# Kernel optimization log

Measured on AMD Instinct MI355X. Metric: run time of the kernel, lower is better.

Reference implementation:

```python
import jax, jax.numpy as jnp
import numpy as np
from jax import lax

DIM = 512; HEADS = 8; HD = DIM // HEADS; SM = 16; NS = 3
B = 8; HH = 32; WW = 32; N = HH * WW; HL = DIM // 4


def setup_inputs() -> dict:
    key = jax.random.key(0)
    ks = iter(jax.random.split(key, 64))
    def g(shape, s=0.02):
        return jax.random.normal(next(ks), shape, dtype=jnp.float32) * s
    z = lambda *sh: jnp.zeros(sh, jnp.float32)
    inp = {
        'x': jax.random.normal(next(ks), (B, N, DIM), dtype=jnp.float32),
        'H': HH, 'W': WW,
        'qkv_w': g((NS, 3 * DIM, DIM)),
        'proj_w': g((DIM, DIM)), 'proj_b': z(DIM),
        'pos_sw': g((HEADS, SM, HD, 2)), 'neg_sw': g((HEADS, SM, HD, 2)),
        'spec_mix': jnp.ones((HEADS, SM), jnp.float32),
        'ca_w1': g((DIM // 2, DIM)), 'ca_b1': z(DIM // 2),
        'ca_w2': g((HEADS * 4, DIM // 2)), 'ca_b2': z(HEADS * 4),
        'lstm_wih_f': g((4 * HL, DIM)), 'lstm_whh_f': g((4 * HL, HL)),
        'lstm_bih_f': z(4 * HL), 'lstm_bhh_f': z(4 * HL),
        'lstm_wih_b': g((4 * HL, DIM)), 'lstm_whh_b': g((4 * HL, HL)),
        'lstm_bih_b': z(4 * HL), 'lstm_bhh_b': z(4 * HL),
        'mha_in_w': g((3 * DIM, DIM)), 'mha_in_b': z(3 * DIM),
        'mha_out_w': g((DIM, DIM)), 'mha_out_b': z(DIM),
        'ge_w1': g((DIM // 2, DIM)), 'ge_b1': z(DIM // 2),
        'ge_w2': g((HEADS * 2, DIM // 2)), 'ge_b2': z(HEADS * 2),
        'spw': jnp.ones((NS, HEADS, HD), jnp.float32),
        'dwc_w5': g((HD, 1, 5, 5), 0.05), 'dwc_b5': z(HD),
        'dwc_w7': g((HD, 1, 7, 7), 0.05), 'dwc_b7': z(HD),
        'dwc_w9': g((HD, 1, 9, 9), 0.05), 'dwc_b9': z(HD),
        'mode_w': jnp.ones((3,), jnp.float32) / 3.0,
    }
    return inp


def reference(x, H, W, qkv_w, proj_w, proj_b, pos_sw, neg_sw, spec_mix,
              ca_w1, ca_b1, ca_w2, ca_b2,
              lstm_wih_f, lstm_whh_f, lstm_bih_f, lstm_bhh_f,
              lstm_wih_b, lstm_whh_b, lstm_bih_b, lstm_bhh_b,
              mha_in_w, mha_in_b, mha_out_w, mha_out_b,
              ge_w1, ge_b1, ge_w2, ge_b2, spw,
              dwc_w5, dwc_b5, dwc_w7, dwc_b7, dwc_w9, dwc_b9, mode_w):
    Bn, Nn, C = x.shape
    heads = HEADS; hd = C // heads

    # ---------- DynamicContextEncoder ----------
    def lstm_dir(xs, wih, whh, bih, bhh):
        # xs: (N, B, C); PyTorch gate order i,f,g,o
        gates_x = xs @ wih.T + (bih + bhh)
        hdim = whh.shape[1]
        def step(carry, gx):
            h, c = carry
            gi = gx + h @ whh.T
            i, f, gg, o = jnp.split(gi, 4, axis=-1)
            c = jax.nn.sigmoid(f) * c + jax.nn.sigmoid(i) * jnp.tanh(gg)
            h = jax.nn.sigmoid(o) * jnp.tanh(c)
            return (h, c), h
        z0 = jnp.zeros((xs.shape[1], hdim), xs.dtype)
        _, hs = lax.scan(step, (z0, z0), gates_x)
        return hs

    xs = jnp.swapaxes(x, 0, 1)  # (N, B, C)
    h_f = lstm_dir(xs, lstm_wih_f, lstm_whh_f, lstm_bih_f, lstm_bhh_f)
    h_b = lstm_dir(xs[::-1], lstm_wih_b, lstm_whh_b, lstm_bih_b, lstm_bhh_b)[::-1]
    local_ctx = jnp.concatenate([h_f, h_b], -1).mean(0)  # (B, dim//2)
    local_ctx = jnp.pad(local_ctx, ((0, 0), (0, C - local_ctx.shape[1])))

    nh2 = heads // 2; hd2 = C // nh2
    qkv_c = x @ mha_in_w.T + mha_in_b
    qc, kc, vc = jnp.split(qkv_c, 3, -1)
    sh = lambda t: t.reshape(Bn, Nn, nh2, hd2).transpose(0, 2, 1, 3)
    qc, kc, vc = sh(qc), sh(kc), sh(vc)
    attn = jax.nn.softmax(jnp.einsum('bhnd,bhmd->bhnm', qc, kc) / float(np.sqrt(hd2)), -1)
    ac = jnp.einsum('bhnm,bhmd->bhnd', attn, vc).transpose(0, 2, 1, 3).reshape(Bn, Nn, C)
    ac = ac @ mha_out_w.T + mha_out_b
    combined = x.mean(1) + local_ctx + ac.mean(1)
    coeffs = jax.nn.sigmoid(jax.nn.relu(combined @ ca_w1.T + ca_b1) @ ca_w2.T + ca_b2)
    coeffs = coeffs.reshape(Bn, heads, 4)

    # ---------- GradientInformedMixer coefficients (x_grad is zeros) ----------
    gz = jnp.zeros((Bn, C), x.dtype)
    gmix = jax.nn.softmax((jnp.tanh(gz @ ge_w1.T + ge_b1) @ ge_w2.T + ge_b2).reshape(Bn, heads, 2), -1)

    # ---------- SpectralPolarityMixer ----------
    smix = jax.nn.softmax(spec_mix, -1).mean(-1)[None, :, None, None]  # per-head scalar
    wp = (pos_sw[..., 0] + 1j * pos_sw[..., 1])[:, :SM, :SM]
    wn = (neg_sw[..., 0] + 1j * neg_sw[..., 1])[:, :SM, :SM]

    def spectral(t):
        tf = jnp.fft.rfft2(t)[:, :, :SM, :SM]
        tp = jnp.fft.irfft2(tf * wp[None], s=(Nn, hd))
        tn = jnp.fft.irfft2(tf * wn[None], s=(Nn, hd))
        return tp + tn * smix

    def safe_pow(t, p):  # relu(t)**p with safe grads
        tp = jnp.where(t > 0, t, 1.0)
        return jnp.where(t > 0, tp ** p, 0.0)

    mw = jax.nn.softmax(mode_w, 0)
    def dwc(xi, w, b):
        return lax.conv_general_dilated(xi, w, (1, 1), 'SAME',
                                        feature_group_count=xi.shape[1],
                                        dimension_numbers=('NCHW', 'OIHW', 'NCHW')) + b[None, :, None, None]

    c0, c1, c2, c3 = [coeffs[:, :, i][:, :, None, None] for i in range(4)]
    g0, g1 = gmix[:, :, 0][:, :, None, None], gmix[:, :, 1][:, :, None, None]

    outs = []
    for s in range(NS):
        qkv = (x @ qkv_w[s].T).reshape(Bn, Nn, 3, heads, hd).transpose(2, 0, 3, 1, 4)
        q, k, v = qkv[0], qkv[1], qkv[2]  # (B, heads, N, hd)
        q = spectral(q); k = spectral(k)
        p = (1.0 + jnp.abs(spw[s]))[None, :, None, :]
        q_pos = safe_pow(q, p); q_neg = safe_pow(-q, p)
        k_pos = safe_pow(k, p); k_neg = safe_pow(-k, p)
        kvpp = jnp.einsum('bhnd,bhne->bhde', k_pos, v)
        kvnn = jnp.einsum('bhnd,bhne->bhde', k_neg, v)
        z = (jnp.einsum('bhnd,bhd->bhn', q_pos, k_pos.sum(2))
             + jnp.einsum('bhnd,bhd->bhn', q_neg, k_neg.sum(2)) + 1e-6)[..., None]
        same = (c0 * jnp.einsum('bhnd,bhde->bhne', q_pos, kvpp)
                + c1 * jnp.einsum('bhnd,bhde->bhne', q_neg, kvnn)) / z
        opp = (c2 * jnp.einsum('bhnd,bhde->bhne', q_pos, kvnn)
               + c3 * jnp.einsum('bhnd,bhde->bhne', q_neg, kvpp)) / z
        mixed = g0 * same + g1 * opp
        v_img = v.reshape(Bn * heads, H, W, hd).transpose(0, 3, 1, 2)
        vcv = mw[0] * dwc(v_img, dwc_w5, dwc_b5) + mw[1] * dwc(v_img, dwc_w7, dwc_b7) + mw[2] * dwc(v_img, dwc_w9, dwc_b9)
        vcv = vcv.transpose(0, 2, 3, 1).reshape(Bn, heads, Nn, hd)
        outs.append(mixed + vcv)

    out = jnp.stack(outs).mean(0).transpose(0, 2, 1, 3).reshape(Bn, Nn, C)
    return out @ proj_w.T + proj_b
```

## Files before the change

kernel.cpp:

```cpp
#include <hip/hip_runtime.h>
#include <hip/hip_bf16.h>
#include <math.h>

typedef __bf16 bf16x8 __attribute__((ext_vector_type(8)));
typedef __bf16 bf16x4 __attribute__((ext_vector_type(4)));
typedef float  f32x4  __attribute__((ext_vector_type(4)));
typedef const float __attribute__((address_space(1)))* gf1p;

#define MFMA(a,b,c) __builtin_amdgcn_mfma_f32_16x16x32_bf16(a, b, c, 0, 0, 0)
#define LOG2E 1.4426950408889634f

static constexpr size_t OFF_R0    = 0;
static constexpr size_t OFF_GXT   = 12582912;
static constexpr size_t OFF_ACCUM = OFF_GXT;
static constexpr size_t OFF_FINAL = OFF_GXT + 4194304;
static constexpr size_t SOFF      = OFF_GXT + 8388608;
static constexpr size_t OFF_ROWSUM= SOFF;
static constexpr size_t OFF_COLW  = OFF_ROWSUM + 32768;
static constexpr size_t OFF_BM    = OFF_COLW;
static constexpr size_t OFF_XPART = OFF_COLW + 327680;
static constexpr size_t OFF_ACM   = OFF_COLW + 524288;
static constexpr size_t OFF_XMEAN = OFF_ACM + 4096;
static constexpr size_t OFF_LC    = OFF_XMEAN + 4096;
static constexpr size_t OFF_COEF  = OFF_LC + 2048;
static constexpr size_t OFF_GMIX  = OFF_COEF + 256;
static constexpr size_t OFF_MW    = OFF_GMIX + 16;
static constexpr size_t OFF_CONV9 = OFF_MW + 4;
static constexpr size_t OFF_CBIAS = OFF_CONV9 + 5184;
static constexpr size_t OFF_WEFF  = OFF_CBIAS + 64;
static constexpr size_t OFF_PPOW  = OFF_WEFF + 4096;
static constexpr size_t OFF_LBIAS = OFF_PPOW + 1536;
static constexpr size_t OFF_W2    = OFF_LBIAS + 1024;
static constexpr size_t OFF_W1CS  = OFF_W2 + 2048;
static constexpr size_t OFF_W1T   = OFF_W1CS + 16384;
static constexpr size_t OFF_HB    = OFF_W1T + 16384;
static constexpr size_t OFF_XB    = OFF_FINAL;
static constexpr size_t OFF_QW    = OFF_FINAL + 2097152;
static constexpr size_t OFF_MW2   = OFF_FINAL + 3276800;
static constexpr size_t OFF_WFB   = OFF_FINAL + 3670016;
static constexpr size_t OFF_WBB   = OFF_FINAL + 3801088;
static constexpr size_t OFF_PWB   = OFF_FINAL + 3932160;

__device__ __forceinline__ float sigm(float x){ return __builtin_amdgcn_rcpf(1.0f + exp2f(-LOG2E*x)); }
__device__ __forceinline__ float tanhx(float x){ return 2.0f*__builtin_amdgcn_rcpf(1.0f + exp2f(-2.0f*LOG2E*x)) - 1.0f; }
__device__ __forceinline__ unsigned pk2(float a, float b){
  union { __bf16 h[2]; unsigned u; } z; z.h[0]=(__bf16)a; z.h[1]=(__bf16)b; return z.u;
}
__device__ __forceinline__ unsigned pk2b(__bf16 a, __bf16 b){
  union { __bf16 h[2]; unsigned u; } z; z.h[0]=a; z.h[1]=b; return z.u;
}
__device__ __forceinline__ void powpair(float t, float p, float& pos, float& neg){
  float a = fabsf(t);
  float v = (a > 0.f) ? exp2f(p * __log2f(a)) : 0.f;
  pos = (t > 0.f) ? v : 0.f;
  neg = (t < 0.f) ? v : 0.f;
}
__device__ __forceinline__ f32x4 fz4(){ return (f32x4){0.f,0.f,0.f,0.f}; }

__global__ void k_cvt_all(const float* __restrict__ x, const float* __restrict__ qkv_w,
                          const float* __restrict__ mha_in_w, const float* __restrict__ wih_f,
                          const float* __restrict__ wih_b, const float* __restrict__ proj_w,
                          float* __restrict__ ws){
  int b = blockIdx.x;
  const float* src; __bf16* dst; int base;
  if (b < 2048){      src=x;        dst=(__bf16*)(ws+OFF_XB);  base=b; }
  else if (b < 3200){ src=qkv_w;    dst=(__bf16*)(ws+OFF_QW);  base=b-2048; }
  else if (b < 3584){ src=mha_in_w; dst=(__bf16*)(ws+OFF_MW2); base=b-3200; }
  else if (b < 3712){ src=wih_f;    dst=(__bf16*)(ws+OFF_WFB); base=b-3584; }
  else if (b < 3840){ src=wih_b;    dst=(__bf16*)(ws+OFF_WBB); base=b-3712; }
  else {              src=proj_w;   dst=(__bf16*)(ws+OFF_PWB); base=b-3840; }
  int i = (base*256 + threadIdx.x)*8;
  f32x4 u0 = *(const f32x4*)(src+i), u1 = *(const f32x4*)(src+i+4);
  bf16x8 v;
  #pragma unroll
  for (int j=0;j<4;++j){ v[j]=(__bf16)u0[j]; v[j+4]=(__bf16)u1[j]; }
  *(bf16x8*)(dst+i) = v;
}

__global__ void k_const(const float* __restrict__ ge_b1, const float* __restrict__ ge_w2,
                        const float* __restrict__ ge_b2, const float* __restrict__ mode_w,
                        const float* __restrict__ w5, const float* __restrict__ b5,
                        const float* __restrict__ w7, const float* __restrict__ b7,
                        const float* __restrict__ w9, const float* __restrict__ b9,
                        const float* __restrict__ pos_sw, const float* __restrict__ neg_sw,
                        const float* __restrict__ spw,
                        const float* __restrict__ bih_f, const float* __restrict__ bhh_f,
                        const float* __restrict__ bih_b, const float* __restrict__ bhh_b,
                        float* __restrict__ ws){
  int tid = threadIdx.x;
  __shared__ float mw[3];
  __shared__ float tgh[256];
  __shared__ float sbuf[16];
  tgh[tid] = tanhf(ge_b1[tid]);
  if (tid == 0){
    float m0=mode_w[0], m1=mode_w[1], m2=mode_w[2];
    float mx = fmaxf(m0, fmaxf(m1,m2));
    float e0=expf(m0-mx), e1=expf(m1-mx), e2=expf(m2-mx);
    float s = e0+e1+e2;
    mw[0]=e0/s; mw[1]=e1/s; mw[2]=e2/s;
    ws[OFF_MW+0]=mw[0]; ws[OFF_MW+1]=mw[1]; ws[OFF_MW+2]=mw[2];
  }
  __syncthreads();
  if (tid < 16){
    float s = ge_b2[tid];
    for (int i=0;i<256;++i) s += ge_w2[tid*256+i]*tgh[i];
    sbuf[tid] = s;
  }
  __syncthreads();
  if (tid < 8){
    float a = sbuf[2*tid], b = sbuf[2*tid+1];
    float m = fmaxf(a,b);
    float ea = expf(a-m), eb = expf(b-m);
    ws[OFF_GMIX+2*tid]   = ea/(ea+eb);
    ws[OFF_GMIX+2*tid+1] = eb/(ea+eb);
  }
  for (int j=tid;j<512;j+=256){
    ws[OFF_LBIAS+j]     = bih_f[j]+bhh_f[j];
    ws[OFF_LBIAS+512+j] = bih_b[j]+bhh_b[j];
  }
  for (int f=tid; f<5184; f+=256){
    int d=f/81, t=f%81, ky=t/9, kx=t%9, dy=ky-4, dx=kx-4;
    float v = mw[2]*w9[d*81+t];
    if (dy>=-3 && dy<=3 && dx>=-3 && dx<=3) v += mw[1]*w7[d*49 + (dy+3)*7 + (dx+3)];
    if (dy>=-2 && dy<=2 && dx>=-2 && dx<=2) v += mw[0]*w5[d*25 + (dy+2)*5 + (dx+2)];
    ws[OFF_CONV9+f] = v;
  }
  if (tid<64) ws[OFF_CBIAS+tid] = mw[0]*b5[tid]+mw[1]*b7[tid]+mw[2]*b9[tid];
  for (int f=tid; f<2048; f+=256){
    int h=f>>8, k1=(f>>4)&15, k2=f&15;
    int src = ((h*16+k1)*64 + k2)*2;
    ws[OFF_WEFF+2*f]   = pos_sw[src]   + 0.0625f*neg_sw[src];
    ws[OFF_WEFF+2*f+1] = pos_sw[src+1] + 0.0625f*neg_sw[src+1];
  }
  for (int f=tid; f<1536; f+=256) ws[OFF_PPOW+f] = 1.0f + fabsf(spw[f]);
  for (int f=tid; f<1024; f+=256){
    int e=f>>4, k2=f&15; int ph=(e*k2)&63;
    float th = (float)ph * (6.283185307179586f/64.0f);
    ws[OFF_W2+2*f]   = cosf(th);
    ws[OFF_W2+2*f+1] = -sinf(th);
  }
  __bf16* w1cs = (__bf16*)(ws + OFF_W1CS);
  for (int f=tid; f<32768; f+=256){
    int r=f>>10, m=f&1023; int k1=r&15; int ph=(k1*m)&1023;
    float th = (float)ph * (6.283185307179586f/1024.0f);
    w1cs[f] = (__bf16)((r<16)?cosf(th):-sinf(th));
  }
  __bf16* w1t = (__bf16*)(ws + OFF_W1T);
  for (int f=tid; f<32768; f+=256){
    int n=f>>5, r=f&31; int k1=r&15; int ph=(k1*n)&1023;
    float th = (float)ph * (6.283185307179586f/1024.0f);
    w1t[f] = (__bf16)((r<16)?cosf(th):sinf(th));
  }
}

template<typename CT>
__global__ __launch_bounds__(256,2) void k_gemm_bf(const __bf16* __restrict__ A, const __bf16* __restrict__ W,
                                                   const float* __restrict__ bias, CT* __restrict__ C,
                                                   int NB_N, int N, int K){
  __shared__ __bf16 As[128][40];
  __shared__ __bf16 Ws[128][40];
  int tid = threadIdx.x;
  int nwg = gridDim.x, o = blockIdx.x;
  int cpx = nwg >> 3;
  int wg = (o & 7)*cpx + (o >> 3);
  int n0 = (wg % NB_N) * 128, m0 = (wg / NB_N) * 128;
  int l = tid & 63, wid = tid >> 6, lr = l & 15, lg = l >> 4;
  int wr = wid >> 1, wc = wid & 1;
  f32x4 acc[4][4];
  #pragma unroll
  for (int i=0;i<4;++i){ acc[i][0]=fz4(); acc[i][1]=fz4(); acc[i][2]=fz4(); acc[i][3]=fz4(); }
  int srow = tid >> 1, sk = (tid & 1) * 16;
  const __bf16* Ap = A + (size_t)(m0 + srow) * K + sk;
  const __bf16* Wp = W + (size_t)(n0 + srow) * K + sk;
  for (int k0 = 0; k0 < K; k0 += 32){
    bf16x8 a0 = *(const bf16x8*)(Ap), a1 = *(const bf16x8*)(Ap+8);
    bf16x8 w0 = *(const bf16x8*)(Wp), w1 = *(const bf16x8*)(Wp+8);
    Ap += 32; Wp += 32;
    __syncthreads();
    *(bf16x8*)&As[srow][sk]   = a0;  *(bf16x8*)&As[srow][sk+8] = a1;
    *(bf16x8*)&Ws[srow][sk]   = w0;  *(bf16x8*)&Ws[srow][sk+8] = w1;
    __syncthreads();
    bf16x8 aF[4], bF[4];
    #pragma unroll
    for (int mf=0;mf<4;++mf) aF[mf] = *(const bf16x8*)&As[wr*64+mf*16+lr][lg*8];
    #pragma unroll
    for (int nf=0;nf<4;++nf) bF[nf] = *(const bf16x8*)&Ws[wc*64+nf*16+lr][lg*8];
    #pragma unroll
    for (int mf=0;mf<4;++mf)
      #pragma unroll
      for (int nf=0;nf<4;++nf) acc[mf][nf] = MFMA(aF[mf], bF[nf], acc[mf][nf]);
  }
  #pragma unroll
  for (int mf=0;mf<4;++mf)
    #pragma unroll
    for (int nf=0;nf<4;++nf){
      int row = m0 + wr*64 + mf*16 + lg*4;
      int col = n0 + wc*64 + nf*16 + lr;
      float bv = bias ? bias[col] : 0.f;
      #pragma unroll
      for (int r=0;r<4;++r) C[(size_t)(row+r)*N + col] = (CT)(acc[mf][nf][r] + bv);
    }
}

__global__ __launch_bounds__(256,2) void k_gemm_acc(const float* __restrict__ accum, const __bf16* __restrict__ W,
                                                    const float* __restrict__ bias, float* __restrict__ C){
  const int N = 512, K = 512, NB_N = 4;
  __shared__ __bf16 As[128][40];
  __shared__ __bf16 Ws[128][40];
  int tid = threadIdx.x;
  int nwg = gridDim.x, o = blockIdx.x;
  int cpx = nwg >> 3;
  int wg = (o & 7)*cpx + (o >> 3);
  int n0 = (wg % NB_N) * 128, m0 = (wg / NB_N) * 128;
  int l = tid & 63, wid = tid >> 6, lr = l & 15, lg = l >> 4;
  int wr = wid >> 1, wc = wid & 1;
  f32x4 acc[4][4];
  #pragma unroll
  for (int i=0;i<4;++i){ acc[i][0]=fz4(); acc[i][1]=fz4(); acc[i][2]=fz4(); acc[i][3]=fz4(); }
  int srow = tid >> 1, sk = (tid & 1) * 16;
  int row = m0 + srow;
  int bb = row >> 10, nn = row & 1023;
  const float* Abase = accum + ((size_t)bb*8192 + nn)*64;
  const __bf16* Wp = W + (size_t)(n0 + srow) * K + sk;
  const float s3 = 1.0f/3.0f;
  for (int k0 = 0; k0 < K; k0 += 32){
    int c0 = k0 + sk;
    const float* Ap = Abase + (size_t)(c0>>6)*65536 + (c0&63);
    f32x4 a0=*(const f32x4*)(Ap), a1=*(const f32x4*)(Ap+4), a2=*(const f32x4*)(Ap+8), a3=*(const f32x4*)(Ap+12);
    bf16x8 w0 = *(const bf16x8*)(Wp), w1 = *(const bf16x8*)(Wp+8);
    Wp += 32;
    __syncthreads();
    bf16x8 va, vb;
    #pragma unroll
    for (int j=0;j<4;++j){ va[j]=(__bf16)(a0[j]*s3); va[j+4]=(__bf16)(a1[j]*s3);
                           vb[j]=(__bf16)(a2[j]*s3); vb[j+4]=(__bf16)(a3[j]*s3); }
    *(bf16x8*)&As[srow][sk]   = va;  *(bf16x8*)&As[srow][sk+8] = vb;
    *(bf16x8*)&Ws[srow][sk]   = w0;  *(bf16x8*)&Ws[srow][sk+8] = w1;
    __syncthreads();
    bf16x8 aF[4], bF[4];
    #pragma unroll
    for (int mf=0;mf<4;++mf) aF[mf] = *(const bf16x8*)&As[wr*64+mf*16+lr][lg*8];
    #pragma unroll
    for (int nf=0;nf<4;++nf) bF[nf] = *(const bf16x8*)&Ws[wc*64+nf*16+lr][lg*8];
    #pragma unroll
    for (int mf=0;mf<4;++mf)
      #pragma unroll
      for (int nf=0;nf<4;++nf) acc[mf][nf] = MFMA(aF[mf], bF[nf], acc[mf][nf]);
  }
  #pragma unroll
  for (int mf=0;mf<4;++mf)
    #pragma unroll
    for (int nf=0;nf<4;++nf){
      int orow = m0 + wr*64 + mf*16 + lg*4;
      int col = n0 + wc*64 + nf*16 + lr;
      float bv = bias[col];
      #pragma unroll
      for (int r=0;r<4;++r) C[(size_t)(orow+r)*N + col] = acc[mf][nf][r] + bv;
    }
}

__global__ __launch_bounds__(256,1) void k_lstm_scan(const float* __restrict__ whh_f,
                                                     const float* __restrict__ whh_b,
                                                     const float* __restrict__ gates,
                                                     float* __restrict__ lc){
  int dir = blockIdx.x >> 3, b = blockIdx.x & 7;
  const float* __restrict__ whh = dir ? whh_b : whh_f;
  const float* gx0 = gates + (size_t)dir*4194304 + (size_t)b*524288;
  gf1p gx1 = (gf1p)(unsigned long long)gx0;
  int tid=threadIdx.x, w=tid>>6, l=tid&63;
  int lr=l&15, lg=l>>4;
  bf16x8 wf[4][2][4];
  #pragma unroll
  for (int q=0;q<4;++q)
    #pragma unroll
    for (int t=0;t<2;++t)
      #pragma unroll
      for (int kc=0;kc<4;++kc){
        const float* p = whh + (size_t)(q*128 + w*32 + t*16 + lr)*128 + kc*32 + lg*8;
        bf16x8 v;
        #pragma unroll
        for (int j=0;j<8;++j) v[j]=(__bf16)p[j];
        wf[q][t][kc]=v;
      }
  __shared__ __bf16 hbuf[2][132];
  for (int i=tid; i<264; i+=256) ((__bf16*)hbuf)[i] = (__bf16)0.0f;
  int tsel = l&1, rsel = (l>>1)&3;
  int hrow = w*32 + tsel*16 + lg*4 + rsel;
  long toff = (dir ? (long)1023*512 : 0) + hrow;
  long tstride = dir ? -512 : 512;
  float cs=0.f, hs=0.f;
  float g0[4], g1[4], g2[4], g3[4];
  #pragma unroll
  for (int q=0;q<4;++q) g0[q] = gx1[toff + q*128];
  toff += tstride;
  #pragma unroll
  for (int q=0;q<4;++q) g1[q] = gx1[toff + q*128];
  toff += tstride;
  #pragma unroll
  for (int q=0;q<4;++q) g2[q] = gx1[toff + q*128];
  toff += tstride;
  #pragma unroll
  for (int q=0;q<4;++q) g3[q] = gx1[toff + q*128];
  toff += tstride;
  __syncthreads();

#define LSTM_STEP(RB, WB, G) { \
    float gq[4]; \
    _Pragma("unroll") for (int q=0;q<4;++q) gq[q]=G[q]; \
    _Pragma("unroll") for (int q=0;q<4;++q) G[q] = gx1[toff + q*128]; \
    toff += tstride; \
    bf16x8 hf[4]; \
    _Pragma("unroll") for (int kc=0;kc<4;++kc) hf[kc] = *(const bf16x8*)&hbuf[RB][kc*32 + lg*8]; \
    f32x4 acc[4][2]; \
    _Pragma("unroll") for (int q=0;q<4;++q){ acc[q][0]=fz4(); acc[q][1]=fz4(); } \
    _Pragma("unroll") for (int kc=0;kc<4;++kc) \
      _Pragma("unroll") for (int q=0;q<4;++q){ \
        acc[q][0] = MFMA(wf[q][0][kc], hf[kc], acc[q][0]); \
        acc[q][1] = MFMA(wf[q][1][kc], hf[kc], acc[q][1]); } \
    float gv[4]; \
    _Pragma("unroll") for (int q=0;q<4;++q){ \
      f32x4 v0 = acc[q][0], v1 = acc[q][1]; \
      float a01 = (rsel&1) ? v0[1] : v0[0]; \
      float a23 = (rsel&1) ? v0[3] : v0[2]; \
      float av  = (rsel&2) ? a23 : a01; \
      float b01 = (rsel&1) ? v1[1] : v1[0]; \
      float b23 = (rsel&1) ? v1[3] : v1[2]; \
      float bv  = (rsel&2) ? b23 : b01; \
      gv[q] = (tsel ? bv : av) + gq[q]; } \
    float ii=sigm(gv[0]), ff=sigm(gv[1]), gg=tanhx(gv[2]), oo=sigm(gv[3]); \
    cs = ff*cs + ii*gg; \
    float hv = oo*tanhx(cs); \
    hs += hv; \
    if (!(l&8)) hbuf[WB][hrow] = (__bf16)hv; \
    asm volatile("s_waitcnt lgkmcnt(0)" ::: "memory"); \
    __builtin_amdgcn_sched_barrier(0); \
    __builtin_amdgcn_s_barrier(); \
    __builtin_amdgcn_sched_barrier(0); }

  for (int it=0; it<256; ++it){
    LSTM_STEP(0, 1, g0)
    LSTM_STEP(1, 0, g1)
    LSTM_STEP(0, 1, g2)
    LSTM_STEP(1, 0, g3)
  }
#undef LSTM_STEP
  if (!(l&8)) lc[b*256 + dir*128 + hrow] = hs*(1.f/1024.f);
}

template<int MODE>
__global__ __launch_bounds__(256,1) void k_mha(const __bf16* __restrict__ qkv, float* __restrict__ rowsum,
                                               float* __restrict__ colw){
  int rb = blockIdx.x, h2 = blockIdx.y, b = blockIdx.z;
  __shared__ __bf16 Qs[256][136];
  __shared__ __bf16 Ks[128][136];
  int tid=threadIdx.x, l=tid&63, w=tid>>6, lr=l&15, lg=l>>4;
  {
    const float qs = LOG2E / sqrtf(128.0f);
    int row = tid;
    const __bf16* p = qkv + ((size_t)(b*1024 + rb*256 + row))*1536 + h2*128;
    #pragma unroll
    for (int cc=0; cc<128; cc+=8){
      bf16x8 u = *(const bf16x8*)(p+cc);
      bf16x8 v;
      #pragma unroll
      for (int j=0;j<8;++j) v[j]=(__bf16)((float)u[j]*qs);
      *(bf16x8*)&Qs[row][cc] = v;
    }
  }
  float rs[4][4];
  if (MODE==1){
    #pragma unroll
    for (int mf=0;mf<4;++mf){ rs[mf][0]=0.f; rs[mf][1]=0.f; rs[mf][2]=0.f; rs[mf][3]=0.f; }
  } else {
    #pragma unroll
    for (int mf=0;mf<4;++mf)
      #pragma unroll
      for (int r=0;r<4;++r)
        rs[mf][r] = 1.0f / rowsum[((size_t)(b*4+h2))*1024 + rb*256 + w*64 + mf*16 + lg*4 + r];
  }
  for (int mc=0; mc<8; ++mc){
    __syncthreads();
    {
      int row = tid>>1, co = (tid&1)*64;
      const __bf16* p = qkv + ((size_t)(b*1024 + mc*128 + row))*1536 + 512 + h2*128 + co;
      #pragma unroll
      for (int cc=0; cc<64; cc+=8)
        *(bf16x8*)&Ks[row][co+cc] = *(const bf16x8*)(p+cc);
    }
    __syncthreads();
    f32x4 acc[4][8];
    #pragma unroll
    for (int mf=0;mf<4;++mf)
      #pragma unroll
      for (int nf=0;nf<8;++nf) acc[mf][nf]=fz4();
    #pragma unroll
    for (int ks=0;ks<4;++ks){
      bf16x8 aF[4], bFv[8];
      #pragma unroll
      for (int mf=0;mf<4;++mf) aF[mf] = *(const bf16x8*)&Qs[w*64+mf*16+lr][ks*32+lg*8];
      #pragma unroll
      for (int nf=0;nf<8;++nf) bFv[nf] = *(const bf16x8*)&Ks[nf*16+lr][ks*32+lg*8];
      #pragma unroll
      for (int mf=0;mf<4;++mf)
        #pragma unroll
        for (int nf=0;nf<8;++nf) acc[mf][nf] = MFMA(aF[mf], bFv[nf], acc[mf][nf]);
    }
    if (MODE==1){
      #pragma unroll
      for (int mf=0;mf<4;++mf)
        #pragma unroll
        for (int nf=0;nf<8;++nf)
          #pragma unroll
          for (int r=0;r<4;++r) rs[mf][r] += exp2f(acc[mf][nf][r]);
    } else {
      #pragma unroll
      for (int nf=0;nf<8;++nf){
        float cv = 0.f;
        #pragma unroll
        for (int mf=0;mf<4;++mf)
          #pragma unroll
          for (int r=0;r<4;++r) cv += exp2f(acc[mf][nf][r])*rs[mf][r];
        cv += __shfl_xor(cv,16);
        cv += __shfl_xor(cv,32);
        if (lg==0)
          colw[(((size_t)(rb*4+w)*8 + b)*4 + h2)*1024 + mc*128 + nf*16 + lr] = cv;
      }
    }
  }
  if (MODE==1){
    #pragma unroll
    for (int mf=0;mf<4;++mf)
      #pragma unroll
      for (int r=0;r<4;++r){
        float v = rs[mf][r];
        v += __shfl_xor(v,1); v += __shfl_xor(v,2); v += __shfl_xor(v,4); v += __shfl_xor(v,8);
        if (lr==0) rowsum[((size_t)(b*4+h2))*1024 + rb*256 + w*64 + mf*16 + lg*4 + r] = v;
      }
  }
}

__global__ void k_mha3(const __bf16* __restrict__ qkv, const float* __restrict__ colw, float* __restrict__ acm){
  int h2 = blockIdx.x & 3, b = blockIdx.x >> 2;
  int tid = threadIdx.x;
  __shared__ float cwred[1024];
  for (int m=tid; m<1024; m+=256){
    float cw=0.f;
    #pragma unroll
    for (int t16=0;t16<16;++t16) cw += colw[(((size_t)t16*8 + b)*4 + h2)*1024 + m];
    cwred[m]=cw;
  }
  __syncthreads();
  int e = tid & 127, half = tid >> 7;
  float s = 0.f;
  for (int m = half*512; m < half*512+512; ++m)
    s += cwred[m] * (float)qkv[((size_t)(b*1024+m))*1536 + 1024 + h2*128 + e];
  __shared__ float red[256];
  red[tid]=s; __syncthreads();
  if (tid<128) acm[((size_t)(b*4+h2))*128 + e] = (red[tid]+red[tid+128])*(1.f/1024.f);
}

__global__ void k_xmean1(const float* __restrict__ x, float* __restrict__ xpart){
  int sl = blockIdx.x, b = blockIdx.y;
  int tid = threadIdx.x;
  #pragma unroll
  for (int cc=0; cc<2; ++cc){
    int c = tid + cc*256;
    float s=0.f;
    for (int n=sl*64; n<sl*64+64; ++n) s += x[((size_t)(b*1024+n))*512 + c];
    xpart[((size_t)(b*16+sl))*512 + c] = s;
  }
}

__global__ __launch_bounds__(256) void k_coeffs(float* __restrict__ ws,
                        const float* __restrict__ mow, const float* __restrict__ mob,
                        const float* __restrict__ ca_w1, const float* __restrict__ ca_b1,
                        const float* __restrict__ ca_w2, const float* __restrict__ ca_b2){
  int b = blockIdx.x, tid = threadIdx.x;
  __shared__ float av[512], comb[512], hid[256];
  for (int i=tid;i<512;i+=256) av[i] = ws[OFF_ACM + b*512 + i];
  __syncthreads();
  for (int c=tid;c<512;c+=256){
    float s = mob[c];
    for (int k=0;k<512;++k) s += mow[(size_t)c*512+k]*av[k];
    float xm = 0.f;
    #pragma unroll
    for (int sl=0; sl<16; ++sl) xm += ws[OFF_XPART + ((size_t)(b*16+sl))*512 + c];
    comb[c] = s + xm*(1.f/1024.f) + ((c<256) ? ws[OFF_LC + b*256 + c] : 0.f);
  }
  __syncthreads();
  for (int j=tid;j<256;j+=256){
    float s = ca_b1[j];
    for (int k=0;k<512;++k) s += ca_w1[(size_t)j*512+k]*comb[k];
    hid[j] = fmaxf(s,0.f);
  }
  __syncthreads();
  if (tid<32){
    float s = ca_b2[tid];
    for (int k=0;k<256;++k) s += ca_w2[tid*256+k]*hid[k];
    ws[OFF_COEF + b*32 + tid] = 1.f/(1.f+expf(-s));
  }
}

__global__ __launch_bounds__(256,1) void k_spec(__bf16* __restrict__ qkv, const float* __restrict__ ws){
  int qk = blockIdx.x, h = blockIdx.y, b = blockIdx.z;
  int colbase = qk*512 + h*64;
  int tid=threadIdx.x, l=tid&63, w=tid>>6, lr=l&15, lg=l>>4;
  __shared__ __bf16 tT[64][520];
  __shared__ float M1[32][64];
  __shared__ float G2[256][2];
  __shared__ __bf16 hbl[2048];
  const __bf16* w1cs = (const __bf16*)(ws + OFF_W1CS);
  f32x4 acc1[2]; acc1[0]=fz4(); acc1[1]=fz4();
  for (int c0=0; c0<2; ++c0){
    __syncthreads();
    {
      int p = tid;
      int m0 = c0*512 + 2*p;
      const __bf16* r0 = qkv + ((size_t)(b*1024 + m0))*1536 + colbase;
      const __bf16* r1 = r0 + 1536;
      #pragma unroll
      for (int e=0;e<64;e+=8){
        bf16x8 u0 = *(const bf16x8*)(r0+e);
        bf16x8 u1 = *(const bf16x8*)(r1+e);
        #pragma unroll
        for (int j=0;j<8;++j) *(unsigned*)&tT[e+j][2*p] = pk2b(u0[j], u1[j]);
      }
    }
    __syncthreads();
    for (int ks=0; ks<16; ++ks){
      bf16x8 bfv = *(const bf16x8*)&tT[w*16+lr][ks*32+lg*8];
      #pragma unroll
      for (int mf=0;mf<2;++mf){
        bf16x8 af = *(const bf16x8*)(w1cs + (size_t)(mf*16+lr)*1024 + c0*512 + ks*32 + lg*8);
        acc1[mf] = MFMA(af, bfv, acc1[mf]);
      }
    }
  }
  #pragma unroll
  for (int mf=0;mf<2;++mf)
    #pragma unroll
    for (int r=0;r<4;++r) M1[mf*16 + lg*4 + r][w*16 + lr] = acc1[mf][r];
  __syncthreads();
  {
    int k1 = tid>>4, k2 = tid&15;
    float tfr=0.f, tfi=0.f;
    const float* w2 = ws + OFF_W2;
    for (int e=0;e<64;++e){
      float mr = M1[k1][e], mi = M1[16+k1][e];
      float cr = w2[(e*16+k2)*2], ci = w2[(e*16+k2)*2+1];
      tfr += mr*cr - mi*ci;
      tfi += mr*ci + mi*cr;
    }
    float wr = ws[OFF_WEFF + ((size_t)h*256 + k1*16 + k2)*2];
    float wi = ws[OFF_WEFF + ((size_t)h*256 + k1*16 + k2)*2 + 1];
    G2[tid][0] = tfr*wr - tfi*wi;
    G2[tid][1] = tfr*wi + tfi*wr;
  }
  __syncthreads();
  {
    const float* w2 = ws + OFF_W2;
    for (int f=tid; f<1024; f+=256){
      int k1 = f>>6, d = f&63;
      float hr=0.f, hi=0.f;
      #pragma unroll
      for (int k2=0;k2<16;++k2){
        float gr=G2[k1*16+k2][0], gi=G2[k1*16+k2][1];
        float sc = k2 ? 2.f : 1.f;
        float cr = sc*w2[(d*16+k2)*2];
        float ci = -sc*w2[(d*16+k2)*2+1];
        hr += gr*cr - gi*ci;
        hi += gr*ci + gi*cr;
      }
      const float inv = 1.0f/65536.0f;
      hbl[d*32 + k1]      = (__bf16)(hr*inv);
      hbl[d*32 + 16 + k1] = (__bf16)(-hi*inv);
    }
  }
  __syncthreads();
  const __bf16* w1t = (const __bf16*)(ws + OFF_W1T);
  bf16x8 bF[4];
  #pragma unroll
  for (int nf=0;nf<4;++nf) bF[nf] = *(const bf16x8*)&hbl[(nf*16+lr)*32 + lg*8];
  for (int pass=0; pass<4; ++pass){
    int rowbase = w*256 + pass*64;
    f32x4 acc[4][4];
    #pragma unroll
    for (int mf=0;mf<4;++mf){ acc[mf][0]=fz4(); acc[mf][1]=fz4(); acc[mf][2]=fz4(); acc[mf][3]=fz4(); }
    #pragma unroll
    for (int mf=0;mf<4;++mf){
      bf16x8 aF = *(const bf16x8*)(w1t + (size_t)(rowbase+mf*16+lr)*32 + lg*8);
      #pragma unroll
      for (int nf=0;nf<4;++nf) acc[mf][nf] = MFMA(aF, bF[nf], acc[mf][nf]);
    }
    #pragma unroll
    for (int mf=0;mf<4;++mf)
      #pragma unroll
      for (int nf=0;nf<4;++nf)
        #pragma unroll
        for (int r=0;r<4;++r){
          int n = rowbase + mf*16 + lg*4 + r;
          int d = nf*16 + lr;
          qkv[((size_t)(b*1024+n))*1536 + colbase + d] = (__bf16)acc[mf][nf][r];
        }
  }
}

__global__ __launch_bounds__(256,1) void k_polar_kv(const __bf16* __restrict__ qkv, float* __restrict__ ws,
                                                    int s){
  int h = blockIdx.x, b = blockIdx.y;
  int tid=threadIdx.x, l=tid&63, w=tid>>6, lr=l&15, lg=l>>4;
  __shared__ float plds[23200];
  __bf16* kpT = (__bf16*)plds;
  __bf16* knT = (__bf16*)((char*)plds + 17408);
  __bf16* vT  = (__bf16*)((char*)plds + 34816);
  float* scal = (float*)((char*)plds + 92416);
  float* pvs  = scal + 8;
  if (tid<4)  scal[tid] = ws[OFF_COEF + b*32 + h*4 + tid];
  if (tid==4) scal[4] = ws[OFF_GMIX + 2*h];
  if (tid==5) scal[5] = ws[OFF_GMIX + 2*h+1];
  if (tid<64) pvs[tid] = ws[OFF_PPOW + ((size_t)s*8+h)*64 + tid];
  for (int i=tid; i<16*136; i+=256) vT[64*136 + i] = (__bf16)((i<136)?1.0f:0.0f);
  f32x4 acc[4][5];
  #pragma unroll
  for (int mf=0;mf<4;++mf)
    #pragma unroll
    for (int nf=0;nf<5;++nf) acc[mf][nf]=fz4();
  for (int mc=0;mc<8;++mc){
    __syncthreads();
    #pragma unroll
    for (int it=0; it<16; ++it){
      int flat = tid + 256*it;
      int d = flat & 63, np = flat >> 6;
      int n = mc*128 + 2*np;
      const __bf16* kr = qkv + ((size_t)(b*1024+n))*1536 + 512 + h*64 + d;
      const __bf16* vr = qkv + ((size_t)(b*1024+n))*1536 + 1024 + h*64 + d;
      float p = pvs[d];
      float k0=(float)kr[0], k1=(float)kr[1536];
      float kp0,kn0,kp1,kn1;
      powpair(k0,p,kp0,kn0); powpair(k1,p,kp1,kn1);
      *(unsigned*)&kpT[d*136 + 2*np] = pk2(kp0,kp1);
      *(unsigned*)&knT[d*136 + 2*np] = pk2(kn0,kn1);
      *(unsigned*)&vT [d*136 + 2*np] = pk2b(vr[0], vr[1536]);
    }
    __syncthreads();
    const __bf16* A = (w&2)?knT:kpT;
    int kh = (w&1)*64;
    #pragma unroll
    for (int ks=0;ks<2;++ks){
      bf16x8 aF[4];
      #pragma unroll
      for (int mf=0;mf<4;++mf) aF[mf] = *(const bf16x8*)&A[(mf*16+lr)*136 + kh + ks*32 + lg*8];
      #pragma unroll
      for (int nf=0;nf<5;++nf){
        bf16x8 bFv = *(const bf16x8*)&vT[(nf*16+lr)*136 + kh + ks*32 + lg*8];
        #pragma unroll
        for (int mf=0;mf<4;++mf) acc[mf][nf] = MFMA(aF[mf], bFv, acc[mf][nf]);
      }
    }
  }
  __syncthreads();
  float* kvf = plds;
  if ((w&1)==0){
    int mat = w>>1;
    #pragma unroll
    for (int mf=0;mf<4;++mf)
      #pragma unroll
      for (int nf=0;nf<5;++nf)
        #pragma unroll
        for (int r=0;r<4;++r)
          kvf[((size_t)mat*64 + mf*16+lg*4+r)*80 + nf*16+lr] = acc[mf][nf][r];
  }
  __syncthreads();
  if (w&1){
    int mat = w>>1;
    #pragma unroll
    for (int mf=0;mf<4;++mf)
      #pragma unroll
      for (int nf=0;nf<5;++nf)
        #pragma unroll
        for (int r=0;r<4;++r)
          kvf[((size_t)mat*64 + mf*16+lg*4+r)*80 + nf*16+lr] += acc[mf][nf][r];
  }
  __syncthreads();
  __bf16* bmg = (__bf16*)(ws + OFF_BM) + (size_t)(b*8+h)*10240;
  {
    float c0=scal[0], c1=scal[1], c2=scal[2], c3=scal[3], g0=scal[4], g1=scal[5];
    for (int f=tid; f<80*128; f+=256){
      int e=f>>7, kk=f&127;
      float v;
      if (e<64){
        if (kk<64) v = g0*c0*kvf[kk*80+e] + g1*c2*kvf[(64+kk)*80+e];
        else { int k2=kk-64; v = g0*c1*kvf[(64+k2)*80+e] + g1*c3*kvf[k2*80+e]; }
      } else if (e==64){
        v = (kk<64) ? kvf[kk*80+64] : kvf[(64+(kk-64))*80+64];
      } else v = 0.f;
      bmg[f] = (__bf16)v;
    }
  }
}

__global__ __launch_bounds__(256,1) void k_polar_ap(const __bf16* __restrict__ qkv, const float* __restrict__ ws,
                                                    float* __restrict__ accum, int s){
  int pass = blockIdx.x, h = blockIdx.y, b = blockIdx.z;
  int tid=threadIdx.x, l=tid&63, w=tid>>6, lr=l&15, lg=l>>4;
  __shared__ __bf16 At[256*136];
  __shared__ __bf16 BmL[80*136];
  __shared__ float zb[256];
  __shared__ float pvs[64];
  if (tid<64) pvs[tid] = ws[OFF_PPOW + ((size_t)s*8+h)*64 + tid];
  {
    const __bf16* bmg = (const __bf16*)(ws + OFF_BM) + (size_t)(b*8+h)*10240;
    for (int u=tid; u<80*16; u+=256){
      int e=u>>4, kx=(u&15)*8;
      *(bf16x8*)&BmL[e*136+kx] = *(const bf16x8*)(bmg + e*128 + kx);
    }
  }
  __syncthreads();
  #pragma unroll
  for (int it=0; it<16; ++it){
    int flat = tid + 256*it;
    int row = flat>>4, dg = flat&15;
    int n = pass*256 + row;
    const __bf16* qr = qkv + ((size_t)(b*1024+n))*1536 + h*64 + dg*4;
    bf16x4 u = *(const bf16x4*)qr;
    float qp[4], qn[4];
    #pragma unroll
    for (int j=0;j<4;++j) powpair((float)u[j], pvs[dg*4+j], qp[j], qn[j]);
    *(unsigned*)&At[row*136 + dg*4]        = pk2(qp[0],qp[1]);
    *(unsigned*)&At[row*136 + dg*4+2]      = pk2(qp[2],qp[3]);
    *(unsigned*)&At[row*136 + 64 + dg*4]   = pk2(qn[0],qn[1]);
    *(unsigned*)&At[row*136 + 64 + dg*4+2] = pk2(qn[2],qn[3]);
  }
  __syncthreads();
  bf16x8 bF2[5][4];
  #pragma unroll
  for (int nf=0;nf<5;++nf)
    #pragma unroll
    for (int ks=0;ks<4;++ks) bF2[nf][ks] = *(const bf16x8*)&BmL[(nf*16+lr)*136 + ks*32 + lg*8];
  f32x4 a2[4][5];
  #pragma unroll
  for (int mf=0;mf<4;++mf)
    #pragma unroll
    for (int nf=0;nf<5;++nf) a2[mf][nf]=fz4();
  #pragma unroll
  for (int ks=0;ks<4;++ks){
    bf16x8 aF[4];
    #pragma unroll
    for (int mf=0;mf<4;++mf) aF[mf] = *(const bf16x8*)&At[(w*64+mf*16+lr)*136 + ks*32 + lg*8];
    #pragma unroll
    for (int nf=0;nf<5;++nf)
      #pragma unroll
      for (int mf=0;mf<4;++mf) a2[mf][nf] = MFMA(aF[mf], bF2[nf][ks], a2[mf][nf]);
  }
  if (lr==0){
    #pragma unroll
    for (int mf=0;mf<4;++mf)
      #pragma unroll
      for (int r=0;r<4;++r) zb[w*64 + mf*16 + lg*4 + r] = a2[mf][4][r] + 1e-6f;
  }
  __syncthreads();
  #pragma unroll
  for (int mf=0;mf<4;++mf){
    float rz[4];
    #pragma unroll
    for (int r=0;r<4;++r) rz[r] = 1.0f / zb[w*64 + mf*16 + lg*4 + r];
    #pragma unroll
    for (int nf=0;nf<4;++nf)
      #pragma unroll
      for (int r=0;r<4;++r){
        int n = pass*256 + w*64 + mf*16 + lg*4 + r;
        int e = nf*16 + lr;
        size_t oi = ((size_t)((b*8+h)*1024) + n)*64 + e;
        float v = a2[mf][nf][r]*rz[r];
        if (s==0) accum[oi] = v; else accum[oi] += v;
      }
  }
}

__global__ __launch_bounds__(256,2) void k_conv(const __bf16* __restrict__ qkv, const float* __restrict__ ws,
                                                float* __restrict__ accum){
  int bid = blockIdx.x;
  int sl = bid & 3, h = (bid>>2)&7, b = bid>>5;
  int tid = threadIdx.x;
  __shared__ float vs[1024][16];
  __shared__ float wc[16][81];
  __shared__ float cb[16];
  for (int it=0; it<64; ++it){
    int flat = tid + 256*it;
    int c = flat & 15, pix = flat>>4;
    vs[pix][c] = (float)qkv[((size_t)(b*1024+pix))*1536 + 1024 + h*64 + sl*16 + c];
  }
  for (int f=tid; f<16*81; f+=256) wc[f/81][f%81] = ws[OFF_CONV9 + (size_t)(sl*16 + f/81)*81 + (f%81)];
  if (tid<16) cb[tid] = ws[OFF_CBIAS + sl*16 + tid];
  __syncthreads();
  #pragma unroll
  for (int cc=0; cc<2; ++cc){
    int col = tid + 256*cc;
    int c = col & 15, x = col >> 4;
    float a[32];
    #pragma unroll
    for (int y=0;y<32;++y) a[y]=0.f;
    #pragma unroll
    for (int dx=-4; dx<=4; ++dx){
      int xx = x+dx;
      bool xv = (xx>=0)&&(xx<32);
      float colv[40];
      #pragma unroll
      for (int i=0;i<40;++i){
        int yy = i-4;
        colv[i] = (xv && yy>=0 && yy<32) ? vs[yy*32+xx][c] : 0.f;
      }
      #pragma unroll
      for (int dy=0; dy<9; ++dy){
        float wv = wc[c][dy*9 + dx+4];
        #pragma unroll
        for (int y=0;y<32;++y) a[y] += wv*colv[y+dy];
      }
    }
    float bias = cb[c];
    #pragma unroll
    for (int y=0;y<32;++y){
      size_t oi = ((size_t)((b*8+h)*1024) + y*32 + x)*64 + sl*16 + c;
      accum[oi] += a[y] + bias;
    }
  }
}

extern "C" void kernel_launch(void* const* d_in, const int* in_sizes, int n_in,
                              void* d_out, int out_size, void* d_ws, size_t ws_size,
                              hipStream_t stream){
  const float* x        = (const float*)d_in[0];
  const float* qkv_w    = (const float*)d_in[3];
  const float* proj_w   = (const float*)d_in[4];
  const float* proj_b   = (const float*)d_in[5];
  const float* pos_sw   = (const float*)d_in[6];
  const float* neg_sw   = (const float*)d_in[7];
  const float* ca_w1    = (const float*)d_in[9];
  const float* ca_b1    = (const float*)d_in[10];
  const float* ca_w2    = (const float*)d_in[11];
  const float* ca_b2    = (const float*)d_in[12];
  const float* wih_f    = (const float*)d_in[13];
  const float* whh_f    = (const float*)d_in[14];
  const float* bih_f    = (const float*)d_in[15];
  const float* bhh_f    = (const float*)d_in[16];
  const float* wih_b    = (const float*)d_in[17];
  const float* whh_b    = (const float*)d_in[18];
  const float* bih_b    = (const float*)d_in[19];
  const float* bhh_b    = (const float*)d_in[20];
  const float* mha_in_w = (const float*)d_in[21];
  const float* mha_in_b = (const float*)d_in[22];
  const float* mha_out_w= (const float*)d_in[23];
  const float* mha_out_b= (const float*)d_in[24];
  const float* ge_b1    = (const float*)d_in[26];
  const float* ge_w2    = (const float*)d_in[27];
  const float* ge_b2    = (const float*)d_in[28];
  const float* spw      = (const float*)d_in[29];
  const float* w5 = (const float*)d_in[30]; const float* b5 = (const float*)d_in[31];
  const float* w7 = (const float*)d_in[32]; const float* b7 = (const float*)d_in[33];
  const float* w9 = (const float*)d_in[34]; const float* b9 = (const float*)d_in[35];
  const float* mode_w = (const float*)d_in[36];
  float* ws  = (float*)d_ws;
  float* out = (float*)d_out;
  __bf16* xb   = (__bf16*)(ws + OFF_XB);
  __bf16* qwb  = (__bf16*)(ws + OFF_QW);
  __bf16* mwb  = (__bf16*)(ws + OFF_MW2);
  __bf16* wfb  = (__bf16*)(ws + OFF_WFB);
  __bf16* wbb  = (__bf16*)(ws + OFF_WBB);
  __bf16* pwb  = (__bf16*)(ws + OFF_PWB);
  __bf16* qkvb = (__bf16*)(ws + OFF_R0);

  k_const<<<1,256,0,stream>>>(ge_b1, ge_w2, ge_b2, mode_w, w5,b5,w7,b7,w9,b9,
                              pos_sw, neg_sw, spw, bih_f,bhh_f,bih_b,bhh_b, ws);
  k_cvt_all<<<3968,256,0,stream>>>(x, qkv_w, mha_in_w, wih_f, wih_b, proj_w, ws);
  k_gemm_bf<float><<<256,256,0,stream>>>(xb, wfb, ws+OFF_LBIAS,     ws+OFF_R0,         4, 512, 512);
  k_gemm_bf<float><<<256,256,0,stream>>>(xb, wbb, ws+OFF_LBIAS+512, ws+OFF_R0+4194304, 4, 512, 512);
  k_lstm_scan<<<16,256,0,stream>>>(whh_f, whh_b, ws+OFF_R0, ws+OFF_LC);
  k_gemm_bf<__bf16><<<768,256,0,stream>>>(xb, mwb, mha_in_b, qkvb, 12, 1536, 512);
  k_mha<1><<<dim3(4,4,8),256,0,stream>>>(qkvb, ws+OFF_ROWSUM, ws+OFF_COLW);
  k_mha<2><<<dim3(4,4,8),256,0,stream>>>(qkvb, ws+OFF_ROWSUM, ws+OFF_COLW);
  k_mha3<<<32,256,0,stream>>>(qkvb, ws+OFF_COLW, ws+OFF_ACM);
  k_xmean1<<<dim3(16,8),256,0,stream>>>(x, ws+OFF_XPART);
  k_coeffs<<<8,256,0,stream>>>(ws, mha_out_w, mha_out_b, ca_w1, ca_b1, ca_w2, ca_b2);
  for (int s=0; s<3; ++s){
    k_gemm_bf<__bf16><<<768,256,0,stream>>>(xb, qwb + (size_t)s*786432, nullptr, qkvb, 12, 1536, 512);
    k_spec<<<dim3(2,8,8),256,0,stream>>>(qkvb, ws);
    k_polar_kv<<<dim3(8,8),256,0,stream>>>(qkvb, ws, s);
    k_polar_ap<<<dim3(4,8,8),256,0,stream>>>(qkvb, ws, ws+OFF_ACCUM, s);
    k_conv<<<256,256,0,stream>>>(qkvb, ws, ws+OFF_ACCUM);
  }
  k_gemm_acc<<<256,256,0,stream>>>(ws+OFF_ACCUM, pwb, proj_b, out);
}
```

Baseline: 1.527 ms.

## Fuse LSTM input GEMMs, split mha3 and polar_ap, raise occupancy, vectorise conv loads

Merges the forward and backward LSTM input-projection GEMMs into one launch producing interleaved gates, and updates the scan's indexing to match. Splits the k_mha3 column reduction across 8 sequence slices, with partial sums reduced in k_coeffs. Halves the k_polar_ap tile so it launches twice as many blocks, and raises launch bounds to 2 blocks per CU for spec/polar kernels, shrinking polar_kv LDS. Vectorises the conv kernel's V loads to bf16x8. These target under-filled grids and serial launches, at the cost of more partial-sum traffic and a few more B-fragment LDS reads.

```diff
diff --git a/kernel.cpp b/kernel.cpp
--- a/kernel.cpp
+++ b/kernel.cpp
@@ -16,6 +16,7 @@
 static constexpr size_t OFF_FINAL = OFF_GXT + 4194304;
 static constexpr size_t SOFF      = OFF_GXT + 8388608;
 static constexpr size_t OFF_ROWSUM= SOFF;
+static constexpr size_t OFF_ACMP  = OFF_ROWSUM;
 static constexpr size_t OFF_COLW  = OFF_ROWSUM + 32768;
 static constexpr size_t OFF_BM    = OFF_COLW;
 static constexpr size_t OFF_XPART = OFF_COLW + 327680;
@@ -33,7 +34,6 @@
 static constexpr size_t OFF_W2    = OFF_LBIAS + 1024;
 static constexpr size_t OFF_W1CS  = OFF_W2 + 2048;
 static constexpr size_t OFF_W1T   = OFF_W1CS + 16384;
-static constexpr size_t OFF_HB    = OFF_W1T + 16384;
 static constexpr size_t OFF_XB    = OFF_FINAL;
 static constexpr size_t OFF_QW    = OFF_FINAL + 2097152;
 static constexpr size_t OFF_MW2   = OFF_FINAL + 3276800;
@@ -265,7 +265,7 @@
                                                      float* __restrict__ lc){
   int dir = blockIdx.x >> 3, b = blockIdx.x & 7;
   const float* __restrict__ whh = dir ? whh_b : whh_f;
-  const float* gx0 = gates + (size_t)dir*4194304 + (size_t)b*524288;
+  const float* gx0 = gates + (size_t)b*1048576;
   gf1p gx1 = (gf1p)(unsigned long long)gx0;
   int tid=threadIdx.x, w=tid>>6, l=tid&63;
   int lr=l&15, lg=l>>4;
@@ -286,8 +286,8 @@
   for (int i=tid; i<264; i+=256) ((__bf16*)hbuf)[i] = (__bf16)0.0f;
   int tsel = l&1, rsel = (l>>1)&3;
   int hrow = w*32 + tsel*16 + lg*4 + rsel;
-  long toff = (dir ? (long)1023*512 : 0) + hrow;
-  long tstride = dir ? -512 : 512;
+  long toff = (dir ? (long)1023*1024 : 0) + dir*512 + hrow;
+  long tstride = dir ? -1024 : 1024;
   float cs=0.f, hs=0.f;
   float g0[4], g1[4], g2[4], g3[4];
   #pragma unroll
@@ -309,6 +309,7 @@
     _Pragma("unroll") for (int q=0;q<4;++q) gq[q]=G[q]; \
     _Pragma("unroll") for (int q=0;q<4;++q) G[q] = gx1[toff + q*128]; \
     toff += tstride; \
+    if (toff < 0) toff = 0;   \
     bf16x8 hf[4]; \
     _Pragma("unroll") for (int kc=0;kc<4;++kc) hf[kc] = *(const bf16x8*)&hbuf[RB][kc*32 + lg*8]; \
     f32x4 acc[4][2]; \
@@ -439,24 +440,24 @@
   }
 }
 
-__global__ void k_mha3(const __bf16* __restrict__ qkv, const float* __restrict__ colw, float* __restrict__ acm){
-  int h2 = blockIdx.x & 3, b = blockIdx.x >> 2;
+__global__ void k_mha3(const __bf16* __restrict__ qkv, const float* __restrict__ colw, float* __restrict__ acmp){
+  int h2 = blockIdx.x, b = blockIdx.y, ms = blockIdx.z;
   int tid = threadIdx.x;
-  __shared__ float cwred[1024];
-  for (int m=tid; m<1024; m+=256){
+  __shared__ float cwred[128];
+  if (tid < 128){
     float cw=0.f;
     #pragma unroll
-    for (int t16=0;t16<16;++t16) cw += colw[(((size_t)t16*8 + b)*4 + h2)*1024 + m];
-    cwred[m]=cw;
+    for (int t16=0;t16<16;++t16) cw += colw[(((size_t)t16*8 + b)*4 + h2)*1024 + ms*128 + tid];
+    cwred[tid]=cw;
   }
   __syncthreads();
   int e = tid & 127, half = tid >> 7;
   float s = 0.f;
-  for (int m = half*512; m < half*512+512; ++m)
-    s += cwred[m] * (float)qkv[((size_t)(b*1024+m))*1536 + 1024 + h2*128 + e];
+  for (int ml = half*64; ml < half*64+64; ++ml)
+    s += cwred[ml] * (float)qkv[((size_t)(b*1024 + ms*128 + ml))*1536 + 1024 + h2*128 + e];
   __shared__ float red[256];
   red[tid]=s; __syncthreads();
-  if (tid<128) acm[((size_t)(b*4+h2))*128 + e] = (red[tid]+red[tid+128])*(1.f/1024.f);
+  if (tid<128) acmp[((size_t)(ms*8+b))*512 + h2*128 + e] = red[tid]+red[tid+128];
 }
 
 __global__ void k_xmean1(const float* __restrict__ x, float* __restrict__ xpart){
@@ -477,7 +478,12 @@
                         const float* __restrict__ ca_w2, const float* __restrict__ ca_b2){
   int b = blockIdx.x, tid = threadIdx.x;
   __shared__ float av[512], comb[512], hid[256];
-  for (int i=tid;i<512;i+=256) av[i] = ws[OFF_ACM + b*512 + i];
+  for (int i=tid;i<512;i+=256){
+    float s = 0.f;
+    #pragma unroll
+    for (int ms=0; ms<8; ++ms) s += ws[OFF_ACMP + ((size_t)(ms*8+b))*512 + i];
+    av[i] = s*(1.f/1024.f);
+  }
   __syncthreads();
   for (int c=tid;c<512;c+=256){
     float s = mob[c];
@@ -501,7 +507,7 @@
   }
 }
 
-__global__ __launch_bounds__(256,1) void k_spec(__bf16* __restrict__ qkv, const float* __restrict__ ws){
+__global__ __launch_bounds__(256,2) void k_spec(__bf16* __restrict__ qkv, const float* __restrict__ ws){
   int qk = blockIdx.x, h = blockIdx.y, b = blockIdx.z;
   int colbase = qk*512 + h*64;
   int tid=threadIdx.x, l=tid&63, w=tid>>6, lr=l&15, lg=l>>4;
@@ -605,15 +611,15 @@
   }
 }
 
-__global__ __launch_bounds__(256,1) void k_polar_kv(const __bf16* __restrict__ qkv, float* __restrict__ ws,
+__global__ __launch_bounds__(256,2) void k_polar_kv(const __bf16* __restrict__ qkv, float* __restrict__ ws,
                                                     int s){
   int h = blockIdx.x, b = blockIdx.y;
   int tid=threadIdx.x, l=tid&63, w=tid>>6, lr=l&15, lg=l>>4;
-  __shared__ float plds[23200];
+  __shared__ float plds[14300];
   __bf16* kpT = (__bf16*)plds;
   __bf16* knT = (__bf16*)((char*)plds + 17408);
   __bf16* vT  = (__bf16*)((char*)plds + 34816);
-  float* scal = (float*)((char*)plds + 92416);
+  float* scal = (float*)((char*)plds + 56576);
   float* pvs  = scal + 8;
   if (tid<4)  scal[tid] = ws[OFF_COEF + b*32 + h*4 + tid];
   if (tid==4) scal[4] = ws[OFF_GMIX + 2*h];
@@ -699,13 +705,13 @@
   }
 }
 
-__global__ __launch_bounds__(256,1) void k_polar_ap(const __bf16* __restrict__ qkv, const float* __restrict__ ws,
+__global__ __launch_bounds__(256,2) void k_polar_ap(const __bf16* __restrict__ qkv, const float* __restrict__ ws,
                                                     float* __restrict__ accum, int s){
-  int pass = blockIdx.x, h = blockIdx.y, b = blockIdx.z;
+  int pass8 = blockIdx.x, h = blockIdx.y, b = blockIdx.z;
   int tid=threadIdx.x, l=tid&63, w=tid>>6, lr=l&15, lg=l>>4;
-  __shared__ __bf16 At[256*136];
+  __shared__ __bf16 At[128*136];
   __shared__ __bf16 BmL[80*136];
-  __shared__ float zb[256];
+  __shared__ float zb[128];
   __shared__ float pvs[64];
   if (tid<64) pvs[tid] = ws[OFF_PPOW + ((size_t)s*8+h)*64 + tid];
   {
@@ -717,10 +723,10 @@
   }
   __syncthreads();
   #pragma unroll
-  for (int it=0; it<16; ++it){
+  for (int it=0; it<8; ++it){
     int flat = tid + 256*it;
     int row = flat>>4, dg = flat&15;
-    int n = pass*256 + row;
+    int n = pass8*128 + row;
     const __bf16* qr = qkv + ((size_t)(b*1024+n))*1536 + h*64 + dg*4;
     bf16x4 u = *(const bf16x4*)qr;
     float qp[4], qn[4];
@@ -732,43 +738,40 @@
     *(unsigned*)&At[row*136 + 64 + dg*4+2] = pk2(qn[2],qn[3]);
   }
   __syncthreads();
-  bf16x8 bF2[5][4];
-  #pragma unroll
-  for (int nf=0;nf<5;++nf)
-    #pragma unroll
-    for (int ks=0;ks<4;++ks) bF2[nf][ks] = *(const bf16x8*)&BmL[(nf*16+lr)*136 + ks*32 + lg*8];
-  f32x4 a2[4][5];
-  #pragma unroll
-  for (int mf=0;mf<4;++mf)
+  f32x4 a2[2][5];
+  #pragma unroll
+  for (int mf=0;mf<2;++mf)
     #pragma unroll
     for (int nf=0;nf<5;++nf) a2[mf][nf]=fz4();
   #pragma unroll
   for (int ks=0;ks<4;++ks){
-    bf16x8 aF[4];
-    #pragma unroll
-    for (int mf=0;mf<4;++mf) aF[mf] = *(const bf16x8*)&At[(w*64+mf*16+lr)*136 + ks*32 + lg*8];
-    #pragma unroll
-    for (int nf=0;nf<5;++nf)
-      #pragma unroll
-      for (int mf=0;mf<4;++mf) a2[mf][nf] = MFMA(aF[mf], bF2[nf][ks], a2[mf][nf]);
+    bf16x8 aF[2];
+    #pragma unroll
+    for (int mf=0;mf<2;++mf) aF[mf] = *(const bf16x8*)&At[(w*32+mf*16+lr)*136 + ks*32 + lg*8];
+    #pragma unroll
+    for (int nf=0;nf<5;++nf){
+      bf16x8 bFv = *(const bf16x8*)&BmL[(nf*16+lr)*136 + ks*32 + lg*8];
+      #pragma unroll
+      for (int mf=0;mf<2;++mf) a2[mf][nf] = MFMA(aF[mf], bFv, a2[mf][nf]);
+    }
   }
   if (lr==0){
     #pragma unroll
-    for (int mf=0;mf<4;++mf)
-      #pragma unroll
-      for (int r=0;r<4;++r) zb[w*64 + mf*16 + lg*4 + r] = a2[mf][4][r] + 1e-6f;
-  }
-  __syncthreads();
-  #pragma unroll
-  for (int mf=0;mf<4;++mf){
+    for (int mf=0;mf<2;++mf)
+      #pragma unroll
+      for (int r=0;r<4;++r) zb[w*32 + mf*16 + lg*4 + r] = a2[mf][4][r] + 1e-6f;
+  }
+  __syncthreads();
+  #pragma unroll
+  for (int mf=0;mf<2;++mf){
     float rz[4];
     #pragma unroll
-    for (int r=0;r<4;++r) rz[r] = 1.0f / zb[w*64 + mf*16 + lg*4 + r];
+    for (int r=0;r<4;++r) rz[r] = 1.0f / zb[w*32 + mf*16 + lg*4 + r];
     #pragma unroll
     for (int nf=0;nf<4;++nf)
       #pragma unroll
       for (int r=0;r<4;++r){
-        int n = pass*256 + w*64 + mf*16 + lg*4 + r;
+        int n = pass8*128 + w*32 + mf*16 + lg*4 + r;
         int e = nf*16 + lr;
         size_t oi = ((size_t)((b*8+h)*1024) + n)*64 + e;
         float v = a2[mf][nf][r]*rz[r];
@@ -785,10 +788,13 @@
   __shared__ float vs[1024][16];
   __shared__ float wc[16][81];
   __shared__ float cb[16];
-  for (int it=0; it<64; ++it){
+  #pragma unroll
+  for (int it=0; it<8; ++it){
     int flat = tid + 256*it;
-    int c = flat & 15, pix = flat>>4;
-    vs[pix][c] = (float)qkv[((size_t)(b*1024+pix))*1536 + 1024 + h*64 + sl*16 + c];
+    int pix = flat>>1, cg = (flat&1)*8;
+    bf16x8 u = *(const bf16x8*)(qkv + ((size_t)(b*1024+pix))*1536 + 1024 + h*64 + sl*16 + cg);
+    #pragma unroll
+    for (int j=0;j<8;++j) vs[pix][cg+j] = (float)u[j];
   }
   for (int f=tid; f<16*81; f+=256) wc[f/81][f%81] = ws[OFF_CONV9 + (size_t)(sl*16 + f/81)*81 + (f%81)];
   if (tid<16) cb[tid] = ws[OFF_CBIAS + sl*16 + tid];
@@ -865,27 +871,25 @@
   __bf16* qwb  = (__bf16*)(ws + OFF_QW);
   __bf16* mwb  = (__bf16*)(ws + OFF_MW2);
   __bf16* wfb  = (__bf16*)(ws + OFF_WFB);
-  __bf16* wbb  = (__bf16*)(ws + OFF_WBB);
   __bf16* pwb  = (__bf16*)(ws + OFF_PWB);
   __bf16* qkvb = (__bf16*)(ws + OFF_R0);
 
   k_const<<<1,256,0,stream>>>(ge_b1, ge_w2, ge_b2, mode_w, w5,b5,w7,b7,w9,b9,
                               pos_sw, neg_sw, spw, bih_f,bhh_f,bih_b,bhh_b, ws);
   k_cvt_all<<<3968,256,0,stream>>>(x, qkv_w, mha_in_w, wih_f, wih_b, proj_w, ws);
-  k_gemm_bf<float><<<256,256,0,stream>>>(xb, wfb, ws+OFF_LBIAS,     ws+OFF_R0,         4, 512, 512);
-  k_gemm_bf<float><<<256,256,0,stream>>>(xb, wbb, ws+OFF_LBIAS+512, ws+OFF_R0+4194304, 4, 512, 512);
+  k_gemm_bf<float><<<512,256,0,stream>>>(xb, wfb, ws+OFF_LBIAS, ws+OFF_R0, 8, 1024, 512);
   k_lstm_scan<<<16,256,0,stream>>>(whh_f, whh_b, ws+OFF_R0, ws+OFF_LC);
   k_gemm_bf<__bf16><<<768,256,0,stream>>>(xb, mwb, mha_in_b, qkvb, 12, 1536, 512);
   k_mha<1><<<dim3(4,4,8),256,0,stream>>>(qkvb, ws+OFF_ROWSUM, ws+OFF_COLW);
   k_mha<2><<<dim3(4,4,8),256,0,stream>>>(qkvb, ws+OFF_ROWSUM, ws+OFF_COLW);
-  k_mha3<<<32,256,0,stream>>>(qkvb, ws+OFF_COLW, ws+OFF_ACM);
+  k_mha3<<<dim3(4,8,8),256,0,stream>>>(qkvb, ws+OFF_COLW, ws+OFF_ACMP);
   k_xmean1<<<dim3(16,8),256,0,stream>>>(x, ws+OFF_XPART);
   k_coeffs<<<8,256,0,stream>>>(ws, mha_out_w, mha_out_b, ca_w1, ca_b1, ca_w2, ca_b2);
   for (int s=0; s<3; ++s){
     k_gemm_bf<__bf16><<<768,256,0,stream>>>(xb, qwb + (size_t)s*786432, nullptr, qkvb, 12, 1536, 512);
     k_spec<<<dim3(2,8,8),256,0,stream>>>(qkvb, ws);
     k_polar_kv<<<dim3(8,8),256,0,stream>>>(qkvb, ws, s);
-    k_polar_ap<<<dim3(4,8,8),256,0,stream>>>(qkvb, ws, ws+OFF_ACCUM, s);
+    k_polar_ap<<<dim3(8,8,8),256,0,stream>>>(qkvb, ws, ws+OFF_ACCUM, s);
     k_conv<<<256,256,0,stream>>>(qkvb, ws, ws+OFF_ACCUM);
   }
   k_gemm_acc<<<256,256,0,stream>>>(ws+OFF_ACCUM, pwb, proj_b, out);
```

After: 1.384 ms. 1.1x faster.
